# Kernel tuning notes

Hardware: AMD Instinct MI355X
Metric: run time of the kernel (lower is better)

Reference implementation:

```python
import jax, jax.numpy as jnp
import numpy as np

NUM_HEADS = 16
EPS = 1e-5


def _ln(x, w, b):
    mu = jnp.mean(x, axis=-1, keepdims=True)
    var = jnp.mean((x - mu) ** 2, axis=-1, keepdims=True)
    return (x - mu) * jax.lax.rsqrt(var + EPS) * w + b


def _ada_ln(x, vol, lw, lb, gamma, beta, vs_w, vs_b):
    y = _ln(x, lw, lb)
    # volatility_scale: Linear(1,1) on vol[..., None] -> sigmoid
    vs = jax.nn.sigmoid(vol[..., None] * vs_w + vs_b)  # (B,S,1)
    return y * (1.0 + vs) * gamma + beta


def setup_inputs() -> dict:
    key = jax.random.key(0)
    ks = jax.random.split(key, 20)
    B, S, H = 8, 1024, 1024
    Hf = 4 * H
    Hg = H // 2
    w = lambda k, i, o: jax.random.normal(k, (i, o), jnp.float32) * 0.02
    inp = {
        'x': jax.random.normal(ks[0], (B, S, H), jnp.float32),
        'volatility': jax.random.uniform(ks[1], (B, S), jnp.float32),
        'Wq': w(ks[2], H, H), 'bq': jnp.zeros((H,), jnp.float32),
        'Wk': w(ks[3], H, H), 'bk': jnp.zeros((H,), jnp.float32),
        'Wv': w(ks[4], H, H), 'bv': jnp.zeros((H,), jnp.float32),
        'Wo': w(ks[5], H, H), 'bo': jnp.zeros((H,), jnp.float32),
        'ln1_w': jnp.ones((H,), jnp.float32), 'ln1_b': jnp.zeros((H,), jnp.float32),
        'gamma1': jnp.ones((), jnp.float32), 'beta1': jnp.zeros((), jnp.float32),
        'vs1_w': jnp.float32(0.3), 'vs1_b': jnp.float32(0.0),
        'ffn_w1': w(ks[6], H, Hf), 'ffn_b1': jnp.zeros((Hf,), jnp.float32),
        'ffn_w2': w(ks[7], Hf, H), 'ffn_b2': jnp.zeros((H,), jnp.float32),
        'gate_w1': w(ks[8], H, Hg), 'gate_b1': jnp.zeros((Hg,), jnp.float32),
        'gate_w2': w(ks[9], Hg, H), 'gate_b2': jnp.zeros((H,), jnp.float32),
        'ln2_w': jnp.ones((H,), jnp.float32), 'ln2_b': jnp.zeros((H,), jnp.float32),
        'gamma2': jnp.ones((), jnp.float32), 'beta2': jnp.zeros((), jnp.float32),
        'vs2_w': jnp.float32(0.3), 'vs2_b': jnp.float32(0.0),
    }
    return inp


def reference(x, volatility, Wq, bq, Wk, bk, Wv, bv, Wo, bo,
              ln1_w, ln1_b, gamma1, beta1, vs1_w, vs1_b,
              ffn_w1, ffn_b1, ffn_w2, ffn_b2,
              gate_w1, gate_b1, gate_w2, gate_b2,
              ln2_w, ln2_b, gamma2, beta2, vs2_w, vs2_b):
    B, S, H = x.shape
    nh = NUM_HEADS
    hd = H // nh
    scale = np.sqrt(hd).astype(np.float32)

    # self-attention (eval mode -> dropout is identity)
    Q = (x @ Wq + bq).reshape(B, S, nh, hd)
    K = (x @ Wk + bk).reshape(B, S, nh, hd)
    V = (x @ Wv + bv).reshape(B, S, nh, hd)
    scores = jnp.einsum('bqhd,bkhd->bhqk', Q, K) / scale
    attn = jax.nn.softmax(scores, axis=-1)
    ctx = jnp.einsum('bhqk,bkhd->bqhd', attn, V).reshape(B, S, H)
    attn_out = ctx @ Wo + bo

    x = x + attn_out
    x = _ada_ln(x, volatility, ln1_w, ln1_b, gamma1, beta1, vs1_w, vs1_b)

    # volatility-adaptive FFN (volatility present -> gated path)
    h = jax.nn.gelu(x @ ffn_w1 + ffn_b1, approximate=False)
    ffn_out = h @ ffn_w2 + ffn_b2
    g = jax.nn.sigmoid(jax.nn.relu(x @ gate_w1 + gate_b1) @ gate_w2 + gate_b2)
    ffn_res = ffn_out * g + x * (1.0 - g)

    x = x + ffn_res
    x = _ada_ln(x, volatility, ln2_w, ln2_b, gamma2, beta2, vs2_w, vs2_b)
    return x
```

## Files before the change

kernel.cpp:

```cpp
#include <hip/hip_runtime.h>
#include <hip/hip_bf16.h>
#include <math.h>


#define HDIM 1024
#define NHEAD 16
#define DHEAD 64
#define NBATCH 8
#define NSEQ 1024
#define NTOK (NBATCH * NSEQ)
#define QKVSTR 3072
#define LNEPS 1e-5f
#define LOG2E_8 0.180336880f

using f32x4 = __attribute__((ext_vector_type(4))) float;
using s16x8 = __attribute__((ext_vector_type(8))) short;
using u16x8 = __attribute__((ext_vector_type(8))) unsigned short;

enum { ACT_NONE = 0, ACT_GELU = 1, ACT_RELU = 2, ACT_SIG = 3 };

__device__ inline float bf2f(unsigned short u) {
    union { unsigned u; float f; } t; t.u = ((unsigned)u) << 16; return t.f;
}
__device__ inline unsigned short f2bf(float f) {
    __hip_bfloat16 h = __float2bfloat16(f);
    return *reinterpret_cast<unsigned short*>(&h);
}
__device__ inline float gelu_f(float t) {
    const float u = t * (0.7978845608f + 0.0356774081f * t * t);
    const float e = __expf(2.f * u);
    const float th = 1.f - 2.f / (e + 1.f);
    return 0.5f * t * (1.f + th);
}

#define GLDS16(g, l) __builtin_amdgcn_global_load_lds( \
    (__attribute__((address_space(1))) void*)(g),      \
    (__attribute__((address_space(3))) void*)(l), 16, 0, 0)

__global__ __launch_bounds__(256)
void cast_bf16_k(const float* __restrict__ in, unsigned short* __restrict__ out, int n4)
{
    for (int i = blockIdx.x * 256 + threadIdx.x; i < n4; i += gridDim.x * 256) {
        float4 v = ((const float4*)in)[i];
        ushort4 o;
        o.x = f2bf(v.x); o.y = f2bf(v.y); o.z = f2bf(v.z); o.w = f2bf(v.w);
        ((ushort4*)out)[i] = o;
    }
}

__global__ __launch_bounds__(256)
void concat3_k(const float* __restrict__ a, const float* __restrict__ b,
               const float* __restrict__ c, float* __restrict__ o)
{
    int i = blockIdx.x * 256 + threadIdx.x;
    o[i] = i < 1024 ? a[i] : (i < 2048 ? b[i - 1024] : c[i - 2048]);
}

__global__ __launch_bounds__(256)
void transpose_cast_k(const float* __restrict__ W, unsigned short* __restrict__ Wt,
                      int K, int N)
{
    __shared__ float tile[32][33];
    const int tx = threadIdx.x, ty = threadIdx.y;
    const int k0 = blockIdx.y * 32, n0 = blockIdx.x * 32;
#pragma unroll
    for (int r = 0; r < 32; r += 8)
        tile[ty + r][tx] = W[(size_t)(k0 + ty + r) * N + n0 + tx];
    __syncthreads();
#pragma unroll
    for (int r = 0; r < 32; r += 8)
        Wt[(size_t)(n0 + ty + r) * K + k0 + tx] = f2bf(tile[tx][ty + r]);
}

__global__ __launch_bounds__(256)
void transpose_cast4_k(const float* __restrict__ W0, const float* __restrict__ W1,
                       const float* __restrict__ W2, const float* __restrict__ W3,
                       unsigned short* __restrict__ Wt)
{
    __shared__ float tile[32][33];
    const int z = blockIdx.z;
    const float* W = z == 0 ? W0 : z == 1 ? W1 : z == 2 ? W2 : W3;
    unsigned short* dst = Wt + (size_t)z * HDIM * HDIM;
    const int tx = threadIdx.x, ty = threadIdx.y;
    const int k0 = blockIdx.y * 32, n0 = blockIdx.x * 32;
#pragma unroll
    for (int r = 0; r < 32; r += 8)
        tile[ty + r][tx] = W[(size_t)(k0 + ty + r) * HDIM + n0 + tx];
    __syncthreads();
#pragma unroll
    for (int r = 0; r < 32; r += 8)
        dst[(size_t)(n0 + ty + r) * HDIM + k0 + tx] = f2bf(tile[tx][ty + r]);
}

__global__ __launch_bounds__(256)
void transpose_v_k(const unsigned short* __restrict__ vb, unsigned short* __restrict__ vtb)
{
    __shared__ unsigned short t[64][72];
    const int tid = threadIdx.x;
    const int b = blockIdx.z, h = blockIdx.y;
    const int s0 = blockIdx.x * 64;
    {
        const int r = tid >> 3, c = (tid & 7) * 8;
        *(u16x8*)&t[r][c] =
            *(const u16x8*)&vb[((size_t)(b * NSEQ + s0 + r)) * QKVSTR + h * DHEAD + c];
        *(u16x8*)&t[r + 32][c] =
            *(const u16x8*)&vb[((size_t)(b * NSEQ + s0 + r + 32)) * QKVSTR + h * DHEAD + c];
    }
    __syncthreads();
    {
        const int d = tid & 63, sc = (tid >> 6) * 16;
        u16x8 o0, o1;
#pragma unroll
        for (int i = 0; i < 8; ++i) o0[i] = t[sc + i][d];
#pragma unroll
        for (int i = 0; i < 8; ++i) o1[i] = t[sc + 8 + i][d];
        unsigned short* dst = &vtb[((size_t)((b * NHEAD + h) * DHEAD + d)) * NSEQ + s0 + sc];
        *(u16x8*)dst = o0;
        *(u16x8*)(dst + 8) = o1;
    }
}

template<int BM, int BN, int ACT, bool HAS_ADD, bool OUT_BF>
__global__ __launch_bounds__(512, (BM == 128) ? 4 : 2)
void gemm8_k(const unsigned short* __restrict__ A, const unsigned short* __restrict__ Bt,
             const float* __restrict__ bias, const float* __restrict__ add,
             void* __restrict__ Cv, int M, int N, int K)
{
    extern __shared__ __align__(16) unsigned short lds[];
    constexpr int BK = 64;
    constexpr int WN = (BN == 256) ? 4 : 2;
    constexpr int WM = 8 / WN;
    constexpr int MREP = BM / (WM * 16);
    constexpr int NREP = BN / (WN * 16);
    constexpr int ASZ = BM * BK;
    constexpr int BSZ = BN * BK;
    constexpr int AR = BM / 64;
    constexpr int BR = BN / 64;
    constexpr int VM = AR + BR;
    constexpr int NPH = (BN == 256) ? 4 : 2;
    constexpr int MI_PER = MREP / 2;
    constexpr int NJ_PER = (BN == 256) ? 2 : 4;

    const int tid = threadIdx.x;
    const int lane = tid & 63;
    const int w = tid >> 6;
    const int wr = w / WN;
    const int wc = w % WN;
    const int m0 = blockIdx.y * BM;
    const int n0 = blockIdx.x * BN;
    const int fr = lane & 15;
    const int fo = lane >> 4;

    const int srow = tid >> 3;
    const int sslot = (tid & 7) ^ (srow & 7);
    const size_t a_base = (size_t)(m0 + srow) * K + sslot * 8;
    const size_t b_base = (size_t)(n0 + srow) * K + sslot * 8;

    f32x4 acc[MREP][NREP] = {};

    auto stage = [&](int t) {
        const int buf = t & 1;
        unsigned short* ad = lds + buf * ASZ + w * 512;
        unsigned short* bd = lds + 2 * ASZ + buf * BSZ + w * 512;
        const unsigned short* as_ = A + a_base + (size_t)t * BK;
        const unsigned short* bs_ = Bt + b_base + (size_t)t * BK;
#pragma unroll
        for (int j = 0; j < AR; ++j)
            GLDS16(as_ + (size_t)j * 64 * K, ad + j * 4096);
#pragma unroll
        for (int j = 0; j < BR; ++j)
            GLDS16(bs_ + (size_t)j * 64 * K, bd + j * 4096);
    };

    const int NT = K / BK;
    stage(0);

    for (int t = 0; t < NT; ++t) {
        if (t + 1 < NT) {
            stage(t + 1);
            asm volatile("s_waitcnt vmcnt(%0)" :: "i"(VM) : "memory");
        } else {
            asm volatile("s_waitcnt vmcnt(0)" ::: "memory");
        }
        __builtin_amdgcn_s_barrier();

        const char* Ab = (const char*)(lds + (t & 1) * ASZ);
        const char* Bb = (const char*)(lds + 2 * ASZ + (t & 1) * BSZ);

        s16x8 af[MI_PER][2], bfr[NJ_PER][2];
#pragma unroll
        for (int ph = 0; ph < NPH; ++ph) {
            const int mh = (BN == 256) ? ((ph == 1 || ph == 2) ? 1 : 0) : ph;
            const int nh = (BN == 256) ? (ph >> 1) : 0;
            const bool la = (BN != 256) || (ph != 2);
            const bool lb = (BN == 256) ? ((ph & 1) == 0) : (ph == 0);
            if (la) {
#pragma unroll
                for (int i = 0; i < MI_PER; ++i) {
                    const int row = wr * (BM / WM) + (mh * MI_PER + i) * 16 + fr;
                    const int sw = (row & 7) << 4;
#pragma unroll
                    for (int kk = 0; kk < 2; ++kk)
                        af[i][kk] = *(const s16x8*)(Ab + row * 128 + ((kk * 64 + fo * 16) ^ sw));
                }
            }
            if (lb) {
#pragma unroll
                for (int j = 0; j < NJ_PER; ++j) {
                    const int row = wc * 64 + (nh * NJ_PER + j) * 16 + fr;
                    const int sw = (row & 7) << 4;
#pragma unroll
                    for (int kk = 0; kk < 2; ++kk)
                        bfr[j][kk] = *(const s16x8*)(Bb + row * 128 + ((kk * 64 + fo * 16) ^ sw));
                }
            }
            __builtin_amdgcn_s_setprio(1);
#pragma unroll
            for (int i = 0; i < MI_PER; ++i)
#pragma unroll
                for (int j = 0; j < NJ_PER; ++j)
#pragma unroll
                    for (int kk = 0; kk < 2; ++kk)
                        acc[mh * MI_PER + i][nh * NJ_PER + j] =
                            __builtin_amdgcn_mfma_f32_16x16x32_bf16(
                                af[i][kk], bfr[j][kk],
                                acc[mh * MI_PER + i][nh * NJ_PER + j], 0, 0, 0);
            __builtin_amdgcn_s_setprio(0);
        }
        asm volatile("s_waitcnt lgkmcnt(0)" ::: "memory");
        __builtin_amdgcn_sched_barrier(0);
        __builtin_amdgcn_s_barrier();
    }

    float bv[NREP];
#pragma unroll
    for (int j = 0; j < NREP; ++j)
        bv[j] = bias[n0 + wc * 64 + j * 16 + fr];
#pragma unroll
    for (int i = 0; i < MREP; ++i) {
#pragma unroll
        for (int j = 0; j < NREP; ++j) {
            const int gn = n0 + wc * 64 + j * 16 + fr;
#pragma unroll
            for (int r = 0; r < 4; ++r) {
                const int gm = m0 + wr * (BM / WM) + i * 16 + fo * 4 + r;
                float t = acc[i][j][r] + bv[j];
                if (HAS_ADD) t += add[(size_t)gm * N + gn];
                if (ACT == ACT_GELU)      t = gelu_f(t);
                else if (ACT == ACT_RELU) t = fmaxf(t, 0.f);
                else if (ACT == ACT_SIG)  t = 1.f / (1.f + __expf(-t));
                if (OUT_BF) ((unsigned short*)Cv)[(size_t)gm * N + gn] = f2bf(t);
                else        ((float*)Cv)[(size_t)gm * N + gn] = t;
            }
        }
    }
}

__global__ __launch_bounds__(512, 6)
void attn_k(const unsigned short* __restrict__ QKVb, const unsigned short* __restrict__ Vtb,
            unsigned short* __restrict__ Cb)
{
    __shared__ alignas(16) unsigned short Ks[2][64 * 64];
    __shared__ alignas(16) unsigned short Vs[2][64 * 64];
    __shared__ alignas(16) unsigned short Ps[8][16 * 72];

    const int tid = threadIdx.x;
    const int lane = tid & 63;
    const int wid = tid >> 6;
    const int L = blockIdx.x;
    const int xcd = L & 7, s = L >> 3;
    const int bh = xcd + ((s >> 3) << 3);
    const int qt = s & 7;
    const int b = bh >> 4, h = bh & 15;
    const int q0 = qt * 128 + wid * 16;

    const int kcol = lane & 15;
    const int kofs = (lane >> 4) * 8;
    const size_t qoff = ((size_t)(b * NSEQ + q0 + kcol)) * QKVSTR + h * DHEAD + kofs;
    const s16x8 qf0 = *(const s16x8*)(QKVb + qoff);
    const s16x8 qf1 = *(const s16x8*)(QKVb + qoff + 32);

    f32x4 accO[4] = {};
    float mrow[4] = {-1e30f, -1e30f, -1e30f, -1e30f};
    float lsum[4] = {0.f, 0.f, 0.f, 0.f};

    const int lr = lane >> 3;
    const int swz8 = (((lane & 7) ^ lr)) * 8;
    const size_t kbase  = ((size_t)(b * NSEQ)) * QKVSTR + HDIM + h * DHEAD;
    const size_t vtbase = ((size_t)(bh * DHEAD)) * NSEQ;

    unsigned short* const pw = &Ps[wid][0];
    const int prow = (lane >> 4) * 4;

    auto stage = [&](int kt, int buf) {
        const int rowb = wid * 8;
        GLDS16(QKVb + kbase + (size_t)(kt * 64 + rowb + lr) * QKVSTR + swz8,
               Ks[buf] + rowb * 64);
        GLDS16(Vtb + vtbase + (size_t)(rowb + lr) * NSEQ + kt * 64 + swz8,
               Vs[buf] + rowb * 64);
    };

    stage(0, 0);
    asm volatile("s_waitcnt vmcnt(0)" ::: "memory");
    __syncthreads();

    for (int kt = 0; kt < NSEQ / 64; ++kt) {
        const int cur = kt & 1;
        if (kt + 1 < NSEQ / 64) stage(kt + 1, cur ^ 1);

        f32x4 sa[4];
#pragma unroll
        for (int jt = 0; jt < 4; ++jt) {
            const int kr = jt * 16 + kcol;
            const unsigned swz = ((unsigned)(kr & 7)) << 4;
            const s16x8 kf0 = *(const s16x8*)((const char*)Ks[cur] + kr * 128 + ((kofs * 2) ^ swz));
            const s16x8 kf1 = *(const s16x8*)((const char*)Ks[cur] + kr * 128 + ((64 + kofs * 2) ^ swz));
            f32x4 t = {};
            t = __builtin_amdgcn_mfma_f32_16x16x32_bf16(qf0, kf0, t, 0, 0, 0);
            t = __builtin_amdgcn_mfma_f32_16x16x32_bf16(qf1, kf1, t, 0, 0, 0);
            sa[jt] = t * LOG2E_8;
        }

        float lmax[4];
#pragma unroll
        for (int r = 0; r < 4; ++r)
            lmax[r] = fmaxf(fmaxf(sa[0][r], sa[1][r]), fmaxf(sa[2][r], sa[3][r]));
        const float guard = fmaxf(fmaxf(lmax[0] - mrow[0], lmax[1] - mrow[1]),
                                  fmaxf(lmax[2] - mrow[2], lmax[3] - mrow[3]));
        if (!__all(guard <= 8.f)) {
#pragma unroll
            for (int r = 0; r < 4; ++r) {
                float m = lmax[r];
                m = fmaxf(m, __shfl_xor(m, 1));
                m = fmaxf(m, __shfl_xor(m, 2));
                m = fmaxf(m, __shfl_xor(m, 4));
                m = fmaxf(m, __shfl_xor(m, 8));
                const float mn = fmaxf(mrow[r], m);
                const float corr = exp2f(mrow[r] - mn);
                mrow[r] = mn;
                lsum[r] *= corr;
#pragma unroll
                for (int dt = 0; dt < 4; ++dt) accO[dt][r] *= corr;
            }
        }
#pragma unroll
        for (int r = 0; r < 4; ++r) {
#pragma unroll
            for (int jt = 0; jt < 4; ++jt) {
                const float p = exp2f(sa[jt][r] - mrow[r]);
                pw[(prow + r) * 72 + jt * 16 + kcol] = f2bf(p);
                lsum[r] += p;
            }
        }

#pragma unroll
        for (int kc = 0; kc < 2; ++kc) {
            const s16x8 pa = *(const s16x8*)(pw + kcol * 72 + kc * 32 + kofs);
#pragma unroll
            for (int dt = 0; dt < 4; ++dt) {
                const int dr = dt * 16 + kcol;
                const unsigned swz = ((unsigned)(dr & 7)) << 4;
                const s16x8 vf = *(const s16x8*)((const char*)Vs[cur] + dr * 128 +
                                                 ((kc * 64 + kofs * 2) ^ swz));
                accO[dt] = __builtin_amdgcn_mfma_f32_16x16x32_bf16(pa, vf, accO[dt], 0, 0, 0);
            }
        }

        if (kt + 1 < NSEQ / 64) asm volatile("s_waitcnt vmcnt(0)" ::: "memory");
        __builtin_amdgcn_s_barrier();
    }

#pragma unroll
    for (int r = 0; r < 4; ++r) {
        lsum[r] += __shfl_xor(lsum[r], 1);
        lsum[r] += __shfl_xor(lsum[r], 2);
        lsum[r] += __shfl_xor(lsum[r], 4);
        lsum[r] += __shfl_xor(lsum[r], 8);
    }

    const size_t obase = ((size_t)(b * NSEQ + q0 + prow)) * HDIM + h * DHEAD;
#pragma unroll
    for (int r = 0; r < 4; ++r) {
        const float rl = 1.f / lsum[r];
#pragma unroll
        for (int dt = 0; dt < 4; ++dt)
            Cb[obase + (size_t)r * HDIM + dt * 16 + kcol] = f2bf(accO[dt][r] * rl);
    }
}

template<int MODE, bool WRITE_BF>
__global__ __launch_bounds__(256)
void adaln_k(const float* __restrict__ a, const float* __restrict__ fo,
             const float* __restrict__ g, const float* __restrict__ vol,
             const float* __restrict__ lw, const float* __restrict__ lb,
             const float* __restrict__ gm, const float* __restrict__ bt,
             const float* __restrict__ vsw, const float* __restrict__ vsb,
             float* __restrict__ out, unsigned short* __restrict__ out_bf)
{
    const int tok = blockIdx.x;
    const int tid = threadIdx.x;
    const size_t base = (size_t)tok * HDIM + tid * 4;
    float v[4];
    {
        float4 va = *(const float4*)&a[base];
        if (MODE == 1) {
            float4 vf = *(const float4*)&fo[base];
            float4 vg = *(const float4*)&g[base];
            v[0] = va.x * (2.f - vg.x) + vf.x * vg.x;
            v[1] = va.y * (2.f - vg.y) + vf.y * vg.y;
            v[2] = va.z * (2.f - vg.z) + vf.z * vg.z;
            v[3] = va.w * (2.f - vg.w) + vf.w * vg.w;
        } else {
            v[0] = va.x; v[1] = va.y; v[2] = va.z; v[3] = va.w;
        }
    }
    float sum = v[0] + v[1] + v[2] + v[3];
    float sq  = v[0]*v[0] + v[1]*v[1] + v[2]*v[2] + v[3]*v[3];
#pragma unroll
    for (int off = 32; off > 0; off >>= 1) {
        sum += __shfl_down(sum, off);
        sq  += __shfl_down(sq, off);
    }
    __shared__ float ssum[4], ssq[4];
    const int wid = tid >> 6, lane = tid & 63;
    if (lane == 0) { ssum[wid] = sum; ssq[wid] = sq; }
    __syncthreads();
    const float tsum = ssum[0] + ssum[1] + ssum[2] + ssum[3];
    const float tsq  = ssq[0]  + ssq[1]  + ssq[2]  + ssq[3];
    const float mu   = tsum * (1.f / 1024.f);
    const float var  = tsq * (1.f / 1024.f) - mu * mu;
    const float rstd = rsqrtf(var + LNEPS);
    const float vsv  = 1.f / (1.f + __expf(-(vol[tok] * vsw[0] + vsb[0])));
    const float sca  = (1.f + vsv) * gm[0];
    const float off2 = bt[0];
    const float4 lwv = *(const float4*)&lw[tid * 4];
    const float4 lbv = *(const float4*)&lb[tid * 4];
    float r0 = ((v[0] - mu) * rstd * lwv.x + lbv.x) * sca + off2;
    float r1 = ((v[1] - mu) * rstd * lwv.y + lbv.y) * sca + off2;
    float r2 = ((v[2] - mu) * rstd * lwv.z + lbv.z) * sca + off2;
    float r3 = ((v[3] - mu) * rstd * lwv.w + lbv.w) * sca + off2;
    *(float4*)&out[base] = make_float4(r0, r1, r2, r3);
    if (WRITE_BF) {
        ushort4 ob;
        ob.x = f2bf(r0); ob.y = f2bf(r1); ob.z = f2bf(r2); ob.w = f2bf(r3);
        *(ushort4*)&out_bf[base] = ob;
    }
}

extern "C" void kernel_launch(void* const* d_in, const int* in_sizes, int n_in,
                              void* d_out, int out_size, void* d_ws, size_t ws_size,
                              hipStream_t stream)
{
    (void)in_sizes; (void)n_in; (void)out_size; (void)ws_size;
    const float* x    = (const float*)d_in[0];
    const float* vol  = (const float*)d_in[1];
    const float* Wq   = (const float*)d_in[2];  const float* bq  = (const float*)d_in[3];
    const float* Wk   = (const float*)d_in[4];  const float* bk  = (const float*)d_in[5];
    const float* Wv   = (const float*)d_in[6];  const float* bv  = (const float*)d_in[7];
    const float* Wo   = (const float*)d_in[8];  const float* bo  = (const float*)d_in[9];
    const float* ln1w = (const float*)d_in[10]; const float* ln1b = (const float*)d_in[11];
    const float* gm1  = (const float*)d_in[12]; const float* be1 = (const float*)d_in[13];
    const float* vs1w = (const float*)d_in[14]; const float* vs1b = (const float*)d_in[15];
    const float* fw1  = (const float*)d_in[16]; const float* fb1 = (const float*)d_in[17];
    const float* fw2  = (const float*)d_in[18]; const float* fb2 = (const float*)d_in[19];
    const float* gw1  = (const float*)d_in[20]; const float* gb1 = (const float*)d_in[21];
    const float* gw2  = (const float*)d_in[22]; const float* gb2 = (const float*)d_in[23];
    const float* ln2w = (const float*)d_in[24]; const float* ln2b = (const float*)d_in[25];
    const float* gm2  = (const float*)d_in[26]; const float* be2 = (const float*)d_in[27];
    const float* vs2w = (const float*)d_in[28]; const float* vs2b = (const float*)d_in[29];

    char* w = (char*)d_ws;
    auto MB = [](size_t v) { return v << 20; };
    unsigned short* wtqkv = (unsigned short*)(w + MB(0));
    unsigned short* wto   = (unsigned short*)(w + MB(6));
    unsigned short* wtf1  = (unsigned short*)(w + MB(8));
    unsigned short* wtf2  = (unsigned short*)(w + MB(16));
    unsigned short* wtg1  = (unsigned short*)(w + MB(24));
    unsigned short* wtg2  = (unsigned short*)(w + MB(25));
    unsigned short* xb   = (unsigned short*)(w + MB(26));
    unsigned short* qkvb = (unsigned short*)(w + MB(42));
    unsigned short* vtb  = (unsigned short*)(w + MB(90));
    unsigned short* cxb  = (unsigned short*)(w + MB(106));
    float*          ao   = (float*)(w + MB(122));
    float*          x1   = (float*)(w + MB(42));
    unsigned short* x1b  = (unsigned short*)(w + MB(74));
    unsigned short* hb   = (unsigned short*)(w + MB(90));
    float*          ffn  = (float*)(w + MB(154));
    unsigned short* ghb  = (unsigned short*)(w + MB(26));
    float*          gg   = (float*)(w + MB(90));
    float*          bqkv = (float*)(w + MB(186));

    dim3 blk(256);
    dim3 tb(32, 8);
    transpose_cast4_k<<<dim3(32, 32, 4), tb, 0, stream>>>(Wq, Wk, Wv, Wo, wtqkv);
    transpose_cast_k<<<dim3(4096/32, 1024/32), tb, 0, stream>>>(fw1, wtf1, 1024, 4096);
    transpose_cast_k<<<dim3(1024/32, 4096/32), tb, 0, stream>>>(fw2, wtf2, 4096, 1024);
    transpose_cast_k<<<dim3(512/32, 1024/32),  tb, 0, stream>>>(gw1, wtg1, 1024, 512);
    transpose_cast_k<<<dim3(1024/32, 512/32),  tb, 0, stream>>>(gw2, wtg2, 512, 1024);
    cast_bf16_k<<<2048, blk, 0, stream>>>(x, xb, NTOK * HDIM / 4);
    concat3_k<<<12, blk, 0, stream>>>(bq, bk, bv, bqkv);

    const size_t SH128 = (128 + 128) * 256;
    const size_t SH256 = (256 + 256) * 256;
    gemm8_k<128, 128, ACT_NONE, false, true><<<dim3(24, 64), 512, SH128, stream>>>(
        xb, wtqkv, bqkv, nullptr, qkvb, NTOK, QKVSTR, HDIM);
    transpose_v_k<<<dim3(NSEQ / 64, NHEAD, NBATCH), blk, 0, stream>>>(qkvb + 2048, vtb);
    attn_k<<<dim3(1024), 512, 0, stream>>>(qkvb, vtb, cxb);
    gemm8_k<128, 128, ACT_NONE, true, false><<<dim3(8, 64), 512, SH128, stream>>>(
        cxb, wto, bo, x, ao, NTOK, HDIM, HDIM);
    adaln_k<0, true><<<dim3(NTOK), blk, 0, stream>>>(
        ao, nullptr, nullptr, vol, ln1w, ln1b, gm1, be1, vs1w, vs1b, x1, x1b);
    gemm8_k<256, 256, ACT_GELU, false, true><<<dim3(16, 32), 512, SH256, stream>>>(
        x1b, wtf1, fb1, nullptr, hb, NTOK, 4096, HDIM);
    gemm8_k<128, 128, ACT_NONE, false, false><<<dim3(8, 64), 512, SH128, stream>>>(
        hb, wtf2, fb2, nullptr, ffn, NTOK, HDIM, 4096);
    gemm8_k<128, 128, ACT_RELU, false, true><<<dim3(4, 64), 512, SH128, stream>>>(
        x1b, wtg1, gb1, nullptr, ghb, NTOK, 512, HDIM);
    gemm8_k<128, 128, ACT_SIG, false, false><<<dim3(8, 64), 512, SH128, stream>>>(
        ghb, wtg2, gb2, nullptr, gg, NTOK, HDIM, 512);
    adaln_k<1, false><<<dim3(NTOK), blk, 0, stream>>>(
        x1, ffn, gg, vol, ln2w, ln2b, gm2, be2, vs2w, vs2b, (float*)d_out, nullptr);
}
```

Measured before the change: 455.9 us.

## Add 8-phase pipelined GEMM with 256-row tiles and quad-buffered K-halves

Introduces a new GEMM kernel that uses 256-row M tiles and splits each 64-wide K step into two 32-wide halves held in a four-slot LDS ring. Global-to-LDS loads for upcoming halves are interleaved between MFMA phases with barriers and explicit vmcnt waits, so copies overlap compute. Most GEMMs (QKV, output projection, FFN1, FFN2, gate2) now use it with one block per CU. The aim is more operand reuse per tile and less exposed memory latency, at the cost of lower occupancy, unswizzled LDS layout (possible bank conflicts), and fewer blocks for the smaller GEMMs.

```diff
diff --git a/kernel.cpp b/kernel.cpp
--- a/kernel.cpp
+++ b/kernel.cpp
@@ -36,6 +36,14 @@
 #define GLDS16(g, l) __builtin_amdgcn_global_load_lds( \
     (__attribute__((address_space(1))) void*)(g),      \
     (__attribute__((address_space(3))) void*)(l), 16, 0, 0)
+#define MFMA16(a, b, c) __builtin_amdgcn_mfma_f32_16x16x32_bf16(a, b, c, 0, 0, 0)
+#define BAR() __builtin_amdgcn_s_barrier()
+#define LGKM0() do { asm volatile("s_waitcnt lgkmcnt(0)" ::: "memory"); \
+                     __builtin_amdgcn_sched_barrier(0); } while (0)
+
+template<int N> __device__ __forceinline__ void vmwait() {
+    asm volatile("s_waitcnt vmcnt(%0)" :: "i"(N) : "memory");
+}
 
 __global__ __launch_bounds__(256)
 void cast_bf16_k(const float* __restrict__ in, unsigned short* __restrict__ out, int n4)
@@ -120,26 +128,21 @@
     }
 }
 
-template<int BM, int BN, int ACT, bool HAS_ADD, bool OUT_BF>
-__global__ __launch_bounds__(512, (BM == 128) ? 4 : 2)
-void gemm8_k(const unsigned short* __restrict__ A, const unsigned short* __restrict__ Bt,
-             const float* __restrict__ bias, const float* __restrict__ add,
-             void* __restrict__ Cv, int M, int N, int K)
+template<int BN, int ACT, bool HAS_ADD, bool OUT_BF>
+__global__ __launch_bounds__(512, 1)
+void gemm_ph8_k(const unsigned short* __restrict__ A, const unsigned short* __restrict__ Bt,
+                const float* __restrict__ bias, const float* __restrict__ add,
+                void* __restrict__ Cv, int M, int N, int K)
 {
     extern __shared__ __align__(16) unsigned short lds[];
-    constexpr int BK = 64;
+    constexpr int BM = 256;
     constexpr int WN = (BN == 256) ? 4 : 2;
     constexpr int WM = 8 / WN;
-    constexpr int MREP = BM / (WM * 16);
-    constexpr int NREP = BN / (WN * 16);
-    constexpr int ASZ = BM * BK;
-    constexpr int BSZ = BN * BK;
-    constexpr int AR = BM / 64;
-    constexpr int BR = BN / 64;
-    constexpr int VM = AR + BR;
-    constexpr int NPH = (BN == 256) ? 4 : 2;
-    constexpr int MI_PER = MREP / 2;
-    constexpr int NJ_PER = (BN == 256) ? 2 : 4;
+    constexpr int WROWS = BM / WM;
+    constexpr int WCOLS = BN / WN;
+    constexpr int MREP = WROWS / 16;
+    constexpr int ASLOT = BM * 32;
+    constexpr int BSLOT = BN * 32;
 
     const int tid = threadIdx.x;
     const int lane = tid & 63;
@@ -151,6 +154,199 @@
     const int fr = lane & 15;
     const int fo = lane >> 4;
 
+    const int srow = lane >> 2;
+    const int sk8 = (lane & 3) * 8;
+
+    f32x4 acc[MREP][4] = {};
+
+    auto stA = [&](int t, int kh) {
+        unsigned short* dst = lds + ((2 * t + kh) & 3) * ASLOT + (w * 32) * 32;
+        const unsigned short* src = A + (size_t)(m0 + w * 32 + srow) * K + t * 64 + kh * 32 + sk8;
+        GLDS16(src, dst);
+        GLDS16(src + (size_t)16 * K, dst + 16 * 32);
+    };
+    auto stB = [&](int t, int kh) {
+        unsigned short* base = lds + 4 * ASLOT + ((2 * t + kh) & 3) * BSLOT;
+        if constexpr (BN == 256) {
+            unsigned short* dst = base + (w * 32) * 32;
+            const unsigned short* src = Bt + (size_t)(n0 + w * 32 + srow) * K + t * 64 + kh * 32 + sk8;
+            GLDS16(src, dst);
+            GLDS16(src + (size_t)16 * K, dst + 16 * 32);
+        } else {
+            unsigned short* dst = base + (w * 16) * 32;
+            const unsigned short* src = Bt + (size_t)(n0 + w * 16 + srow) * K + t * 64 + kh * 32 + sk8;
+            GLDS16(src, dst);
+        }
+    };
+
+    const int NT = K / 64;
+    stA(0, 0); stB(0, 0);
+    stA(0, 1); stB(0, 1);
+    stA(1, 0); stB(1, 0);
+    if constexpr (BN == 256) vmwait<8>(); else vmwait<6>();
+    BAR();
+
+    for (int t = 0; t < NT; ++t) {
+        const bool s1 = (t + 1 < NT);
+        const bool s2 = (t + 2 < NT);
+        const int tail = (t == NT - 1) ? 2 : ((t == NT - 2) ? 1 : 0);
+        const int sl0 = (2 * t) & 3;
+        const int sl1 = (2 * t + 1) & 3;
+
+        if constexpr (BN == 256) {
+            s16x8 afr[4], bfr[4];
+#pragma unroll
+            for (int i = 0; i < 4; ++i)
+                afr[i] = *(const s16x8*)(lds + sl0 * ASLOT + (wr * 128 + i * 16 + fr) * 32 + fo * 8);
+#pragma unroll
+            for (int j = 0; j < 4; ++j)
+                bfr[j] = *(const s16x8*)(lds + 4 * ASLOT + sl0 * BSLOT + (wc * 64 + j * 16 + fr) * 32 + fo * 8);
+            if (s1) stA(t + 1, 1);
+            BAR(); LGKM0();
+            __builtin_amdgcn_s_setprio(1);
+#pragma unroll
+            for (int i = 0; i < 4; ++i)
+#pragma unroll
+                for (int j = 0; j < 4; ++j)
+                    acc[i][j] = MFMA16(afr[i], bfr[j], acc[i][j]);
+            __builtin_amdgcn_s_setprio(0);
+            BAR();
+#pragma unroll
+            for (int i = 0; i < 4; ++i)
+                afr[i] = *(const s16x8*)(lds + sl0 * ASLOT + (wr * 128 + 64 + i * 16 + fr) * 32 + fo * 8);
+            if (s1) stB(t + 1, 1);
+            BAR(); LGKM0();
+            __builtin_amdgcn_s_setprio(1);
+#pragma unroll
+            for (int i = 0; i < 4; ++i)
+#pragma unroll
+                for (int j = 0; j < 4; ++j)
+                    acc[4 + i][j] = MFMA16(afr[i], bfr[j], acc[4 + i][j]);
+            __builtin_amdgcn_s_setprio(0);
+            if (tail < 2) vmwait<8>(); else vmwait<0>();
+            BAR();
+#pragma unroll
+            for (int i = 0; i < 4; ++i)
+                afr[i] = *(const s16x8*)(lds + sl1 * ASLOT + (wr * 128 + 64 + i * 16 + fr) * 32 + fo * 8);
+#pragma unroll
+            for (int j = 0; j < 4; ++j)
+                bfr[j] = *(const s16x8*)(lds + 4 * ASLOT + sl1 * BSLOT + (wc * 64 + j * 16 + fr) * 32 + fo * 8);
+            if (s2) stA(t + 2, 0);
+            BAR(); LGKM0();
+            __builtin_amdgcn_s_setprio(1);
+#pragma unroll
+            for (int i = 0; i < 4; ++i)
+#pragma unroll
+                for (int j = 0; j < 4; ++j)
+                    acc[4 + i][j] = MFMA16(afr[i], bfr[j], acc[4 + i][j]);
+            __builtin_amdgcn_s_setprio(0);
+            BAR();
+#pragma unroll
+            for (int i = 0; i < 4; ++i)
+                afr[i] = *(const s16x8*)(lds + sl1 * ASLOT + (wr * 128 + i * 16 + fr) * 32 + fo * 8);
+            if (s2) stB(t + 2, 0);
+            BAR(); LGKM0();
+            __builtin_amdgcn_s_setprio(1);
+#pragma unroll
+            for (int i = 0; i < 4; ++i)
+#pragma unroll
+                for (int j = 0; j < 4; ++j)
+                    acc[i][j] = MFMA16(afr[i], bfr[j], acc[i][j]);
+            __builtin_amdgcn_s_setprio(0);
+            if (tail == 0) vmwait<8>(); else if (tail == 1) vmwait<4>();
+            BAR();
+        } else {
+            s16x8 afr[4], bfr[4];
+#pragma unroll
+            for (int i = 0; i < 4; ++i)
+                afr[i] = *(const s16x8*)(lds + sl0 * ASLOT + (wr * 64 + i * 16 + fr) * 32 + fo * 8);
+#pragma unroll
+            for (int j = 0; j < 4; ++j)
+                bfr[j] = *(const s16x8*)(lds + 4 * ASLOT + sl0 * BSLOT + (wc * 64 + j * 16 + fr) * 32 + fo * 8);
+            if (s1) { stA(t + 1, 1); stB(t + 1, 1); }
+            BAR(); LGKM0();
+            __builtin_amdgcn_s_setprio(1);
+#pragma unroll
+            for (int i = 0; i < 4; ++i)
+#pragma unroll
+                for (int j = 0; j < 4; ++j)
+                    acc[i][j] = MFMA16(afr[i], bfr[j], acc[i][j]);
+            __builtin_amdgcn_s_setprio(0);
+            if (tail < 2) vmwait<6>(); else vmwait<0>();
+            BAR();
+#pragma unroll
+            for (int i = 0; i < 4; ++i)
+                afr[i] = *(const s16x8*)(lds + sl1 * ASLOT + (wr * 64 + i * 16 + fr) * 32 + fo * 8);
+#pragma unroll
+            for (int j = 0; j < 4; ++j)
+                bfr[j] = *(const s16x8*)(lds + 4 * ASLOT + sl1 * BSLOT + (wc * 64 + j * 16 + fr) * 32 + fo * 8);
+            if (s2) { stA(t + 2, 0); stB(t + 2, 0); }
+            BAR(); LGKM0();
+            __builtin_amdgcn_s_setprio(1);
+#pragma unroll
+            for (int i = 0; i < 4; ++i)
+#pragma unroll
+                for (int j = 0; j < 4; ++j)
+                    acc[i][j] = MFMA16(afr[i], bfr[j], acc[i][j]);
+            __builtin_amdgcn_s_setprio(0);
+            if (tail == 0) vmwait<6>(); else if (tail == 1) vmwait<3>();
+            BAR();
+        }
+    }
+
+    float bv[4];
+#pragma unroll
+    for (int j = 0; j < 4; ++j)
+        bv[j] = bias[n0 + wc * WCOLS + j * 16 + fr];
+#pragma unroll
+    for (int i = 0; i < MREP; ++i) {
+        const int rbase = (BN == 256) ? ((i >> 2) * 64 + (i & 3) * 16) : (i * 16);
+#pragma unroll
+        for (int j = 0; j < 4; ++j) {
+            const int gn = n0 + wc * WCOLS + j * 16 + fr;
+#pragma unroll
+            for (int r = 0; r < 4; ++r) {
+                const int gm = m0 + wr * WROWS + rbase + fo * 4 + r;
+                float t = acc[i][j][r] + bv[j];
+                if (HAS_ADD) t += add[(size_t)gm * N + gn];
+                if (ACT == ACT_GELU)      t = gelu_f(t);
+                else if (ACT == ACT_RELU) t = fmaxf(t, 0.f);
+                else if (ACT == ACT_SIG)  t = 1.f / (1.f + __expf(-t));
+                if (OUT_BF) ((unsigned short*)Cv)[(size_t)gm * N + gn] = f2bf(t);
+                else        ((float*)Cv)[(size_t)gm * N + gn] = t;
+            }
+        }
+    }
+}
+
+template<int BM, int BN, int ACT, bool HAS_ADD, bool OUT_BF>
+__global__ __launch_bounds__(512, (BM == 128) ? 4 : 2)
+void gemm8_k(const unsigned short* __restrict__ A, const unsigned short* __restrict__ Bt,
+             const float* __restrict__ bias, const float* __restrict__ add,
+             void* __restrict__ Cv, int M, int N, int K)
+{
+    extern __shared__ __align__(16) unsigned short lds[];
+    constexpr int BK = 64;
+    constexpr int WN = 2;
+    constexpr int WM = 4;
+    constexpr int MREP = BM / (WM * 16);
+    constexpr int NREP = BN / (WN * 16);
+    constexpr int ASZ = BM * BK;
+    constexpr int BSZ = BN * BK;
+    constexpr int AR = BM / 64;
+    constexpr int BR = BN / 64;
+    constexpr int VM = AR + BR;
+
+    const int tid = threadIdx.x;
+    const int lane = tid & 63;
+    const int w = tid >> 6;
+    const int wr = w / WN;
+    const int wc = w % WN;
+    const int m0 = blockIdx.y * BM;
+    const int n0 = blockIdx.x * BN;
+    const int fr = lane & 15;
+    const int fo = lane >> 4;
+
     const int srow = tid >> 3;
     const int sslot = (tid & 7) ^ (srow & 7);
     const size_t a_base = (size_t)(m0 + srow) * K + sslot * 8;
@@ -187,27 +383,21 @@
         const char* Ab = (const char*)(lds + (t & 1) * ASZ);
         const char* Bb = (const char*)(lds + 2 * ASZ + (t & 1) * BSZ);
 
-        s16x8 af[MI_PER][2], bfr[NJ_PER][2];
-#pragma unroll
-        for (int ph = 0; ph < NPH; ++ph) {
-            const int mh = (BN == 256) ? ((ph == 1 || ph == 2) ? 1 : 0) : ph;
-            const int nh = (BN == 256) ? (ph >> 1) : 0;
-            const bool la = (BN != 256) || (ph != 2);
-            const bool lb = (BN == 256) ? ((ph & 1) == 0) : (ph == 0);
-            if (la) {
-#pragma unroll
-                for (int i = 0; i < MI_PER; ++i) {
-                    const int row = wr * (BM / WM) + (mh * MI_PER + i) * 16 + fr;
-                    const int sw = (row & 7) << 4;
-#pragma unroll
-                    for (int kk = 0; kk < 2; ++kk)
-                        af[i][kk] = *(const s16x8*)(Ab + row * 128 + ((kk * 64 + fo * 16) ^ sw));
-                }
+        s16x8 af[MREP / 2][2], bfr[NREP][2];
+#pragma unroll
+        for (int ph = 0; ph < 2; ++ph) {
+#pragma unroll
+            for (int i = 0; i < MREP / 2; ++i) {
+                const int row = wr * (BM / WM) + (ph * (MREP / 2) + i) * 16 + fr;
+                const int sw = (row & 7) << 4;
+#pragma unroll
+                for (int kk = 0; kk < 2; ++kk)
+                    af[i][kk] = *(const s16x8*)(Ab + row * 128 + ((kk * 64 + fo * 16) ^ sw));
             }
-            if (lb) {
-#pragma unroll
-                for (int j = 0; j < NJ_PER; ++j) {
-                    const int row = wc * 64 + (nh * NJ_PER + j) * 16 + fr;
+            if (ph == 0) {
+#pragma unroll
+                for (int j = 0; j < NREP; ++j) {
+                    const int row = wc * 64 + j * 16 + fr;
                     const int sw = (row & 7) << 4;
 #pragma unroll
                     for (int kk = 0; kk < 2; ++kk)
@@ -216,15 +406,13 @@
             }
             __builtin_amdgcn_s_setprio(1);
 #pragma unroll
-            for (int i = 0; i < MI_PER; ++i)
-#pragma unroll
-                for (int j = 0; j < NJ_PER; ++j)
+            for (int i = 0; i < MREP / 2; ++i)
+#pragma unroll
+                for (int j = 0; j < NREP; ++j)
 #pragma unroll
                     for (int kk = 0; kk < 2; ++kk)
-                        acc[mh * MI_PER + i][nh * NJ_PER + j] =
-                            __builtin_amdgcn_mfma_f32_16x16x32_bf16(
-                                af[i][kk], bfr[j][kk],
-                                acc[mh * MI_PER + i][nh * NJ_PER + j], 0, 0, 0);
+                        acc[ph * (MREP / 2) + i][j] =
+                            MFMA16(af[i][kk], bfr[j][kk], acc[ph * (MREP / 2) + i][j]);
             __builtin_amdgcn_s_setprio(0);
         }
         asm volatile("s_waitcnt lgkmcnt(0)" ::: "memory");
@@ -316,8 +504,8 @@
             const s16x8 kf0 = *(const s16x8*)((const char*)Ks[cur] + kr * 128 + ((kofs * 2) ^ swz));
             const s16x8 kf1 = *(const s16x8*)((const char*)Ks[cur] + kr * 128 + ((64 + kofs * 2) ^ swz));
             f32x4 t = {};
-            t = __builtin_amdgcn_mfma_f32_16x16x32_bf16(qf0, kf0, t, 0, 0, 0);
-            t = __builtin_amdgcn_mfma_f32_16x16x32_bf16(qf1, kf1, t, 0, 0, 0);
+            t = MFMA16(qf0, kf0, t);
+            t = MFMA16(qf1, kf1, t);
             sa[jt] = t * LOG2E_8;
         }
 
@@ -362,7 +550,7 @@
                 const unsigned swz = ((unsigned)(dr & 7)) << 4;
                 const s16x8 vf = *(const s16x8*)((const char*)Vs[cur] + dr * 128 +
                                                  ((kc * 64 + kofs * 2) ^ swz));
-                accO[dt] = __builtin_amdgcn_mfma_f32_16x16x32_bf16(pa, vf, accO[dt], 0, 0, 0);
+                accO[dt] = MFMA16(pa, vf, accO[dt]);
             }
         }
 
@@ -500,23 +688,25 @@
     cast_bf16_k<<<2048, blk, 0, stream>>>(x, xb, NTOK * HDIM / 4);
     concat3_k<<<12, blk, 0, stream>>>(bq, bk, bv, bqkv);
 
+    const size_t PH256 = 131072;
+    const size_t PH128 = 98304;
     const size_t SH128 = (128 + 128) * 256;
-    const size_t SH256 = (256 + 256) * 256;
-    gemm8_k<128, 128, ACT_NONE, false, true><<<dim3(24, 64), 512, SH128, stream>>>(
+
+    gemm_ph8_k<128, ACT_NONE, false, true><<<dim3(24, 32), 512, PH128, stream>>>(
         xb, wtqkv, bqkv, nullptr, qkvb, NTOK, QKVSTR, HDIM);
     transpose_v_k<<<dim3(NSEQ / 64, NHEAD, NBATCH), blk, 0, stream>>>(qkvb + 2048, vtb);
     attn_k<<<dim3(1024), 512, 0, stream>>>(qkvb, vtb, cxb);
-    gemm8_k<128, 128, ACT_NONE, true, false><<<dim3(8, 64), 512, SH128, stream>>>(
+    gemm_ph8_k<128, ACT_NONE, true, false><<<dim3(8, 32), 512, PH128, stream>>>(
         cxb, wto, bo, x, ao, NTOK, HDIM, HDIM);
     adaln_k<0, true><<<dim3(NTOK), blk, 0, stream>>>(
         ao, nullptr, nullptr, vol, ln1w, ln1b, gm1, be1, vs1w, vs1b, x1, x1b);
-    gemm8_k<256, 256, ACT_GELU, false, true><<<dim3(16, 32), 512, SH256, stream>>>(
+    gemm_ph8_k<256, ACT_GELU, false, true><<<dim3(16, 32), 512, PH256, stream>>>(
         x1b, wtf1, fb1, nullptr, hb, NTOK, 4096, HDIM);
-    gemm8_k<128, 128, ACT_NONE, false, false><<<dim3(8, 64), 512, SH128, stream>>>(
+    gemm_ph8_k<128, ACT_NONE, false, false><<<dim3(8, 32), 512, PH128, stream>>>(
         hb, wtf2, fb2, nullptr, ffn, NTOK, HDIM, 4096);
     gemm8_k<128, 128, ACT_RELU, false, true><<<dim3(4, 64), 512, SH128, stream>>>(
         x1b, wtg1, gb1, nullptr, ghb, NTOK, 512, HDIM);
-    gemm8_k<128, 128, ACT_SIG, false, false><<<dim3(8, 64), 512, SH128, stream>>>(
+    gemm_ph8_k<128, ACT_SIG, false, false><<<dim3(8, 32), 512, PH128, stream>>>(
         ghb, wtg2, gb2, nullptr, gg, NTOK, HDIM, 512);
     adaln_k<1, false><<<dim3(NTOK), blk, 0, stream>>>(
         x1, ffn, gg, vol, ln2w, ln2b, gm2, be2, vs2w, vs2b, (float*)d_out, nullptr);
```

Result: slower. 491.7 us (+7.9%).

## Replace GEMM with 256-thread 128x128 BK=32 kernel and XCD-aware block remap

Applied to the files above, without the earlier changes.

Replaces the templated 512-thread GEMM, which used 128x128 or 256x256 tiles with BK=64, with a single 256-thread kernel using 128x128 tiles, BK=32 and static LDS. Each wave now computes a 64x64 sub-tile. A 1D grid is remapped so consecutive tiles land on the same XCD (chunked by 8), aiming for better L2 reuse. The FFN1 GEMM drops its 256x256 tile, which lowers per-block data reuse, and halving BK doubles the number of barriers per K. In exchange it gets smaller LDS footprint and potentially higher occupancy.

```diff
diff --git a/kernel.cpp b/kernel.cpp
--- a/kernel.cpp
+++ b/kernel.cpp
@@ -36,6 +36,14 @@
 #define GLDS16(g, l) __builtin_amdgcn_global_load_lds( \
     (__attribute__((address_space(1))) void*)(g),      \
     (__attribute__((address_space(3))) void*)(l), 16, 0, 0)
+#define MFMA16(a, b, c) __builtin_amdgcn_mfma_f32_16x16x32_bf16(a, b, c, 0, 0, 0)
+#define BAR() __builtin_amdgcn_s_barrier()
+#define LGKM0() do { asm volatile("s_waitcnt lgkmcnt(0)" ::: "memory"); \
+                     __builtin_amdgcn_sched_barrier(0); } while (0)
+
+template<int N> __device__ __forceinline__ void vmwait() {
+    asm volatile("s_waitcnt vmcnt(%0)" :: "i"(N) : "memory");
+}
 
 __global__ __launch_bounds__(256)
 void cast_bf16_k(const float* __restrict__ in, unsigned short* __restrict__ out, int n4)
@@ -120,130 +128,84 @@
     }
 }
 
-template<int BM, int BN, int ACT, bool HAS_ADD, bool OUT_BF>
-__global__ __launch_bounds__(512, (BM == 128) ? 4 : 2)
-void gemm8_k(const unsigned short* __restrict__ A, const unsigned short* __restrict__ Bt,
-             const float* __restrict__ bias, const float* __restrict__ add,
-             void* __restrict__ Cv, int M, int N, int K)
-{
-    extern __shared__ __align__(16) unsigned short lds[];
-    constexpr int BK = 64;
-    constexpr int WN = (BN == 256) ? 4 : 2;
-    constexpr int WM = 8 / WN;
-    constexpr int MREP = BM / (WM * 16);
-    constexpr int NREP = BN / (WN * 16);
-    constexpr int ASZ = BM * BK;
-    constexpr int BSZ = BN * BK;
-    constexpr int AR = BM / 64;
-    constexpr int BR = BN / 64;
-    constexpr int VM = AR + BR;
-    constexpr int NPH = (BN == 256) ? 4 : 2;
-    constexpr int MI_PER = MREP / 2;
-    constexpr int NJ_PER = (BN == 256) ? 2 : 4;
+template<int ACT, bool HAS_ADD, bool OUT_BF>
+__global__ __launch_bounds__(256, 4)
+void gemm_hi_k(const unsigned short* __restrict__ A, const unsigned short* __restrict__ Bt,
+               const float* __restrict__ bias, const float* __restrict__ add,
+               void* __restrict__ Cv, int M, int N, int K, int nbx)
+{
+    __shared__ alignas(16) unsigned short As[2][128 * 32];
+    __shared__ alignas(16) unsigned short Bs[2][128 * 32];
 
     const int tid = threadIdx.x;
     const int lane = tid & 63;
     const int w = tid >> 6;
-    const int wr = w / WN;
-    const int wc = w % WN;
-    const int m0 = blockIdx.y * BM;
-    const int n0 = blockIdx.x * BN;
+    const int wr = w >> 1, wc = w & 1;
+    const int chunk = gridDim.x >> 3;
+    const int wg = (blockIdx.x & 7) * chunk + (blockIdx.x >> 3);
+    const int m0 = (wg / nbx) * 128;
+    const int n0 = (wg % nbx) * 128;
+
     const int fr = lane & 15;
     const int fo = lane >> 4;
-
-    const int srow = tid >> 3;
-    const int sslot = (tid & 7) ^ (srow & 7);
-    const size_t a_base = (size_t)(m0 + srow) * K + sslot * 8;
-    const size_t b_base = (size_t)(n0 + srow) * K + sslot * 8;
-
-    f32x4 acc[MREP][NREP] = {};
+    const int fo_swz8 = (fo ^ ((fr >> 1) & 3)) * 8;
+
+    const int srow = tid >> 2;
+    const int sg8 = ((tid & 3) ^ ((tid >> 3) & 3)) * 8;
+
+    f32x4 acc[4][4] = {};
 
     auto stage = [&](int t) {
         const int buf = t & 1;
-        unsigned short* ad = lds + buf * ASZ + w * 512;
-        unsigned short* bd = lds + 2 * ASZ + buf * BSZ + w * 512;
-        const unsigned short* as_ = A + a_base + (size_t)t * BK;
-        const unsigned short* bs_ = Bt + b_base + (size_t)t * BK;
-#pragma unroll
-        for (int j = 0; j < AR; ++j)
-            GLDS16(as_ + (size_t)j * 64 * K, ad + j * 4096);
-#pragma unroll
-        for (int j = 0; j < BR; ++j)
-            GLDS16(bs_ + (size_t)j * 64 * K, bd + j * 4096);
+        const unsigned short* as_ = A + (size_t)(m0 + srow) * K + t * 32 + sg8;
+        const unsigned short* bs_ = Bt + (size_t)(n0 + srow) * K + t * 32 + sg8;
+        GLDS16(as_, &As[buf][(w * 16) * 32]);
+        GLDS16(as_ + (size_t)64 * K, &As[buf][(64 + w * 16) * 32]);
+        GLDS16(bs_, &Bs[buf][(w * 16) * 32]);
+        GLDS16(bs_ + (size_t)64 * K, &Bs[buf][(64 + w * 16) * 32]);
     };
 
-    const int NT = K / BK;
+    const int NT = K / 32;
     stage(0);
 
     for (int t = 0; t < NT; ++t) {
-        if (t + 1 < NT) {
-            stage(t + 1);
-            asm volatile("s_waitcnt vmcnt(%0)" :: "i"(VM) : "memory");
-        } else {
-            asm volatile("s_waitcnt vmcnt(0)" ::: "memory");
-        }
-        __builtin_amdgcn_s_barrier();
-
-        const char* Ab = (const char*)(lds + (t & 1) * ASZ);
-        const char* Bb = (const char*)(lds + 2 * ASZ + (t & 1) * BSZ);
-
-        s16x8 af[MI_PER][2], bfr[NJ_PER][2];
-#pragma unroll
-        for (int ph = 0; ph < NPH; ++ph) {
-            const int mh = (BN == 256) ? ((ph == 1 || ph == 2) ? 1 : 0) : ph;
-            const int nh = (BN == 256) ? (ph >> 1) : 0;
-            const bool la = (BN != 256) || (ph != 2);
-            const bool lb = (BN == 256) ? ((ph & 1) == 0) : (ph == 0);
-            if (la) {
-#pragma unroll
-                for (int i = 0; i < MI_PER; ++i) {
-                    const int row = wr * (BM / WM) + (mh * MI_PER + i) * 16 + fr;
-                    const int sw = (row & 7) << 4;
-#pragma unroll
-                    for (int kk = 0; kk < 2; ++kk)
-                        af[i][kk] = *(const s16x8*)(Ab + row * 128 + ((kk * 64 + fo * 16) ^ sw));
-                }
-            }
-            if (lb) {
-#pragma unroll
-                for (int j = 0; j < NJ_PER; ++j) {
-                    const int row = wc * 64 + (nh * NJ_PER + j) * 16 + fr;
-                    const int sw = (row & 7) << 4;
-#pragma unroll
-                    for (int kk = 0; kk < 2; ++kk)
-                        bfr[j][kk] = *(const s16x8*)(Bb + row * 128 + ((kk * 64 + fo * 16) ^ sw));
-                }
-            }
-            __builtin_amdgcn_s_setprio(1);
-#pragma unroll
-            for (int i = 0; i < MI_PER; ++i)
-#pragma unroll
-                for (int j = 0; j < NJ_PER; ++j)
-#pragma unroll
-                    for (int kk = 0; kk < 2; ++kk)
-                        acc[mh * MI_PER + i][nh * NJ_PER + j] =
-                            __builtin_amdgcn_mfma_f32_16x16x32_bf16(
-                                af[i][kk], bfr[j][kk],
-                                acc[mh * MI_PER + i][nh * NJ_PER + j], 0, 0, 0);
-            __builtin_amdgcn_s_setprio(0);
-        }
-        asm volatile("s_waitcnt lgkmcnt(0)" ::: "memory");
-        __builtin_amdgcn_sched_barrier(0);
-        __builtin_amdgcn_s_barrier();
-    }
-
-    float bv[NREP];
-#pragma unroll
-    for (int j = 0; j < NREP; ++j)
+        if (t + 1 < NT) { stage(t + 1); vmwait<4>(); }
+        else            { vmwait<0>(); }
+        BAR();
+
+        const int buf = t & 1;
+        s16x8 af[4], bf[4];
+#pragma unroll
+        for (int i = 0; i < 4; ++i)
+            af[i] = *(const s16x8*)(&As[buf][(wr * 64 + i * 16 + fr) * 32 + fo_swz8]);
+#pragma unroll
+        for (int j = 0; j < 4; ++j)
+            bf[j] = *(const s16x8*)(&Bs[buf][(wc * 64 + j * 16 + fr) * 32 + fo_swz8]);
+
+        __builtin_amdgcn_s_setprio(1);
+#pragma unroll
+        for (int i = 0; i < 4; ++i)
+#pragma unroll
+            for (int j = 0; j < 4; ++j)
+                acc[i][j] = MFMA16(af[i], bf[j], acc[i][j]);
+        __builtin_amdgcn_s_setprio(0);
+
+        LGKM0();
+        BAR();
+    }
+
+    float bv[4];
+#pragma unroll
+    for (int j = 0; j < 4; ++j)
         bv[j] = bias[n0 + wc * 64 + j * 16 + fr];
 #pragma unroll
-    for (int i = 0; i < MREP; ++i) {
-#pragma unroll
-        for (int j = 0; j < NREP; ++j) {
+    for (int i = 0; i < 4; ++i) {
+#pragma unroll
+        for (int j = 0; j < 4; ++j) {
             const int gn = n0 + wc * 64 + j * 16 + fr;
 #pragma unroll
             for (int r = 0; r < 4; ++r) {
-                const int gm = m0 + wr * (BM / WM) + i * 16 + fo * 4 + r;
+                const int gm = m0 + wr * 64 + i * 16 + fo * 4 + r;
                 float t = acc[i][j][r] + bv[j];
                 if (HAS_ADD) t += add[(size_t)gm * N + gn];
                 if (ACT == ACT_GELU)      t = gelu_f(t);
@@ -316,8 +278,8 @@
             const s16x8 kf0 = *(const s16x8*)((const char*)Ks[cur] + kr * 128 + ((kofs * 2) ^ swz));
             const s16x8 kf1 = *(const s16x8*)((const char*)Ks[cur] + kr * 128 + ((64 + kofs * 2) ^ swz));
             f32x4 t = {};
-            t = __builtin_amdgcn_mfma_f32_16x16x32_bf16(qf0, kf0, t, 0, 0, 0);
-            t = __builtin_amdgcn_mfma_f32_16x16x32_bf16(qf1, kf1, t, 0, 0, 0);
+            t = MFMA16(qf0, kf0, t);
+            t = MFMA16(qf1, kf1, t);
             sa[jt] = t * LOG2E_8;
         }
 
@@ -362,7 +324,7 @@
                 const unsigned swz = ((unsigned)(dr & 7)) << 4;
                 const s16x8 vf = *(const s16x8*)((const char*)Vs[cur] + dr * 128 +
                                                  ((kc * 64 + kofs * 2) ^ swz));
-                accO[dt] = __builtin_amdgcn_mfma_f32_16x16x32_bf16(pa, vf, accO[dt], 0, 0, 0);
+                accO[dt] = MFMA16(pa, vf, accO[dt]);
             }
         }
 
@@ -500,24 +462,22 @@
     cast_bf16_k<<<2048, blk, 0, stream>>>(x, xb, NTOK * HDIM / 4);
     concat3_k<<<12, blk, 0, stream>>>(bq, bk, bv, bqkv);
 
-    const size_t SH128 = (128 + 128) * 256;
-    const size_t SH256 = (256 + 256) * 256;
-    gemm8_k<128, 128, ACT_NONE, false, true><<<dim3(24, 64), 512, SH128, stream>>>(
-        xb, wtqkv, bqkv, nullptr, qkvb, NTOK, QKVSTR, HDIM);
+    gemm_hi_k<ACT_NONE, false, true><<<dim3(24 * 64), blk, 0, stream>>>(
+        xb, wtqkv, bqkv, nullptr, qkvb, NTOK, QKVSTR, HDIM, 24);
     transpose_v_k<<<dim3(NSEQ / 64, NHEAD, NBATCH), blk, 0, stream>>>(qkvb + 2048, vtb);
     attn_k<<<dim3(1024), 512, 0, stream>>>(qkvb, vtb, cxb);
-    gemm8_k<128, 128, ACT_NONE, true, false><<<dim3(8, 64), 512, SH128, stream>>>(
-        cxb, wto, bo, x, ao, NTOK, HDIM, HDIM);
+    gemm_hi_k<ACT_NONE, true, false><<<dim3(8 * 64), blk, 0, stream>>>(
+        cxb, wto, bo, x, ao, NTOK, HDIM, HDIM, 8);
     adaln_k<0, true><<<dim3(NTOK), blk, 0, stream>>>(
         ao, nullptr, nullptr, vol, ln1w, ln1b, gm1, be1, vs1w, vs1b, x1, x1b);
-    gemm8_k<256, 256, ACT_GELU, false, true><<<dim3(16, 32), 512, SH256, stream>>>(
-        x1b, wtf1, fb1, nullptr, hb, NTOK, 4096, HDIM);
-    gemm8_k<128, 128, ACT_NONE, false, false><<<dim3(8, 64), 512, SH128, stream>>>(
-        hb, wtf2, fb2, nullptr, ffn, NTOK, HDIM, 4096);
-    gemm8_k<128, 128, ACT_RELU, false, true><<<dim3(4, 64), 512, SH128, stream>>>(
-        x1b, wtg1, gb1, nullptr, ghb, NTOK, 512, HDIM);
-    gemm8_k<128, 128, ACT_SIG, false, false><<<dim3(8, 64), 512, SH128, stream>>>(
-        ghb, wtg2, gb2, nullptr, gg, NTOK, HDIM, 512);
+    gemm_hi_k<ACT_GELU, false, true><<<dim3(32 * 64), blk, 0, stream>>>(
+        x1b, wtf1, fb1, nullptr, hb, NTOK, 4096, HDIM, 32);
+    gemm_hi_k<ACT_NONE, false, false><<<dim3(8 * 64), blk, 0, stream>>>(
+        hb, wtf2, fb2, nullptr, ffn, NTOK, HDIM, 4096, 8);
+    gemm_hi_k<ACT_RELU, false, true><<<dim3(4 * 64), blk, 0, stream>>>(
+        x1b, wtg1, gb1, nullptr, ghb, NTOK, 512, HDIM, 4);
+    gemm_hi_k<ACT_SIG, false, false><<<dim3(8 * 64), blk, 0, stream>>>(
+        ghb, wtg2, gb2, nullptr, gg, NTOK, HDIM, 512, 8);
     adaln_k<1, false><<<dim3(NTOK), blk, 0, stream>>>(
         x1, ffn, gg, vol, ln2w, ln2b, gm2, be2, vs2w, vs2b, (float*)d_out, nullptr);
 }
```

After: 469.4 us. 1.03x slower.
